# Optimization experiments

Measured on AMD Instinct MI355X. Metric: run time of the kernel, lower is better.

## Reference

```python
import jax, jax.numpy as jnp
import numpy as np

EPS = 1e-5  # RMSNorm epsilon


def rmsnorm(x, w):
    return x * jax.lax.rsqrt(jnp.mean(x * x, axis=-1, keepdims=True) + EPS) * w


def mamba_forward(u, in_proj_w, conv_w, conv_b, x_proj_w, dt_proj_w, dt_proj_b,
                  A_log, D_param, mamba_out_w):
    # u: (b, L, dm) -- canonical Mamba block (expand=2, d_state=16, d_conv=4)
    b, L, dm = u.shape
    di, ds = A_log.shape
    dtr = dt_proj_w.shape[1]
    xz = jnp.einsum('bld,ed->ble', u, in_proj_w)          # (b,L,2*di)
    x_, z = jnp.split(xz, 2, axis=-1)                     # each (b,L,di)
    # causal depthwise conv over the sequence axis
    dconv = conv_w.shape[-1]
    xc = jnp.transpose(x_, (0, 2, 1))                     # (b,di,L)
    xc = jnp.pad(xc, ((0, 0), (0, 0), (dconv - 1, 0)))
    xc = jax.lax.conv_general_dilated(xc, conv_w, window_strides=(1,), padding='VALID',
                                      dimension_numbers=('NCH', 'OIH', 'NCH'),
                                      feature_group_count=di)
    xc = xc + conv_b[None, :, None]
    x_ = jax.nn.silu(jnp.transpose(xc, (0, 2, 1)))        # (b,L,di)
    # input-dependent dt, B, C
    x_dbl = jnp.einsum('bld,ed->ble', x_, x_proj_w)       # (b,L,dtr+2*ds)
    dt, B, C = jnp.split(x_dbl, [dtr, dtr + ds], axis=-1)
    delta = jax.nn.softplus(jnp.einsum('blr,dr->bld', dt, dt_proj_w) + dt_proj_b)  # (b,L,di)
    A = -jnp.exp(A_log)                                   # (di,ds)

    def step(h, inp):
        d_t, B_t, C_t, x_t = inp                          # (b,di),(b,ds),(b,ds),(b,di)
        dA = jnp.exp(d_t[:, :, None] * A)                 # (b,di,ds)
        h = dA * h + (d_t * x_t)[:, :, None] * B_t[:, None, :]
        y = jnp.einsum('bds,bs->bd', h, C_t)
        return h, y

    xs = (jnp.moveaxis(delta, 1, 0), jnp.moveaxis(B, 1, 0),
          jnp.moveaxis(C, 1, 0), jnp.moveaxis(x_, 1, 0))
    h0 = jnp.zeros((b, di, ds), dtype=u.dtype)
    _, ys = jax.lax.scan(step, h0, xs)                    # ys: (L,b,di)
    y = jnp.moveaxis(ys, 0, 1) + x_ * D_param             # (b,L,di)
    y = y * jax.nn.silu(z)
    return jnp.einsum('bld,od->blo', y, mamba_out_w)      # (b,L,dm)


def conv1x1(W, bvec, t):
    # t: (b, cin, L) -> (b, cout, L)
    return jnp.einsum('oi,bit->bot', W, t) + bvec[None, :, None]


def reference(x, w_norm1, w_norm2, W_ip, b_ip, W_fp, b_fp, W_wp, b_wp, W_op, b_op,
              in_proj_w, conv_w, conv_b, x_proj_w, dt_proj_w, dt_proj_b,
              A_log, D_param, mamba_out_w):
    # x: (b, L, D) -- module's (b, c, l) with l == input_dim = D, c == seq = L
    residual = x
    xn = rmsnorm(x, w_norm1)                 # RMSNorm over last (input_dim) axis
    xt = jnp.transpose(xn, (0, 2, 1))        # 'b c l -> b l c' : (b, D, L)
    ssm = conv1x1(W_ip, b_ip, xt)            # (b, 2D, L)
    ssm = conv1x1(W_fp, b_fp, ssm)           # (b, 2D, L)
    u = jnp.transpose(ssm, (0, 2, 1))        # (b, L, 2D): seq=L, d_model=2D
    m = mamba_forward(u, in_proj_w, conv_w, conv_b, x_proj_w, dt_proj_w, dt_proj_b,
                      A_log, D_param, mamba_out_w)
    m = rmsnorm(m, w_norm2) + u              # PostNormMamba residual
    ssm = jnp.transpose(m, (0, 2, 1))        # (b, 2D, L)
    w = conv1x1(W_wp, b_wp, xt)              # (b, 2D, L)
    w = w * jax.nn.sigmoid(w)                # swish
    out = conv1x1(W_op, b_op, w * ssm)       # (b, D, L)
    return jnp.transpose(out, (0, 2, 1)) + residual


def setup_inputs():
    key = jax.random.key(0)
    ks = jax.random.split(key, 16)
    D, L, b = 64, 4096, 4
    dm, di, ds, dconv = 2 * D, 4 * D, 16, 4
    dtr = (dm + 15) // 16  # dt_rank = ceil(d_model/16) = 8

    def n(k, shape, fan_in):
        return jax.random.normal(k, shape, jnp.float32) * (1.0 / np.sqrt(fan_in))

    return {
        'x': jax.random.normal(ks[0], (b, L, D), jnp.float32),
        'w_norm1': jnp.ones((D,), jnp.float32),
        'w_norm2': jnp.ones((dm,), jnp.float32),
        'W_ip': n(ks[1], (2 * D, D), D), 'b_ip': jnp.zeros((2 * D,), jnp.float32),
        'W_fp': n(ks[2], (2 * D, 2 * D), 2 * D), 'b_fp': jnp.zeros((2 * D,), jnp.float32),
        'W_wp': n(ks[3], (2 * D, D), D), 'b_wp': jnp.zeros((2 * D,), jnp.float32),
        'W_op': n(ks[4], (D, 2 * D), 2 * D), 'b_op': jnp.zeros((D,), jnp.float32),
        'in_proj_w': n(ks[5], (2 * di, dm), dm),
        'conv_w': n(ks[6], (di, 1, dconv), dconv),
        'conv_b': jnp.zeros((di,), jnp.float32),
        'x_proj_w': n(ks[7], (dtr + 2 * ds, di), di),
        'dt_proj_w': n(ks[8], (di, dtr), dtr),
        'dt_proj_b': jnp.full((di,), float(np.log(np.expm1(0.01))), jnp.float32),
        'A_log': jnp.log(jnp.broadcast_to(jnp.arange(1, ds + 1, dtype=jnp.float32), (di, ds))),
        'D_param': jnp.ones((di,), jnp.float32),
        'mamba_out_w': n(ks[9], (dm, di), di),
    }
```

## Files before the change

### kernel.cpp

```cpp
#include <hip/hip_runtime.h>
#include <hip/hip_bf16.h>

typedef __hip_bfloat16 bf16;
typedef __attribute__((ext_vector_type(8))) short bf16x8;
typedef __attribute__((ext_vector_type(4))) float f32x4;
#define DEV __device__ __forceinline__

constexpr int SEQ  = 4096;
constexpr int NB   = 4;
constexpr int NTOK = NB * SEQ;
constexpr float EPS = 1e-5f;
constexpr int NCH = 64;
constexpr int NCHUNK = SEQ / NCH;
constexpr float LOG2E = 1.44269504f;

constexpr int OFF_WDT  = 0;
constexpr int OFF_WB   = 2048;
constexpr int WB_IP = 0;
constexpr int WB_WP = 8192;
constexpr int WB_FP = 16384;
constexpr int WB_PR = 32768;
constexpr int WB_MO = 98304;
constexpr int WB_OP = 131072;
constexpr int WB_XP = 139264;
constexpr int WB_TOT = 151552;
constexpr int OFF_XDBL = OFF_WB + WB_TOT / 2;
constexpr int OFF_R1   = OFF_XDBL + NTOK * 40;
constexpr int OFF_WSW  = OFF_R1   + 1048576;
constexpr int OFF_U    = OFF_WSW  + 1048576;
constexpr int OFF_R2   = OFF_U    + 1048576;
constexpr int OFF_SILUZ= OFF_R2   + 2097152;
constexpr int OFF_XC   = OFF_SILUZ+ 2097152;
constexpr int OFF_G    = OFF_XC   + 2097152;
constexpr int OFF_FLAG = OFF_G    + 2097152;

DEV float b2f(bf16 x) { return __bfloat162float(x); }
DEV bf16 f2b(float x) { return __float2bfloat16(x); }
DEV short shof(bf16 h) { short s; __builtin_memcpy(&s, &h, 2); return s; }
DEV float ldin(const void* p, int i, int f) {
  return f ? ((const float*)p)[i] : b2f(((const bf16*)p)[i]);
}
DEV unsigned pack2(float a, float b) {
  bf16 ha = f2b(a), hb = f2b(b);
  unsigned short ua, ub;
  __builtin_memcpy(&ua, &ha, 2); __builtin_memcpy(&ub, &hb, 2);
  return (unsigned)ua | ((unsigned)ub << 16);
}
DEV float lo16f(unsigned u) { return __int_as_float((int)(u << 16)); }
DEV float hi16f(unsigned u) { return __int_as_float((int)(u & 0xffff0000u)); }
DEV float exp2f_fast(float a) { return __builtin_amdgcn_exp2f(a); }
DEV float softplus(float a) {
  return (a > 20.f) ? a : __logf(1.f + exp2f_fast(a * LOG2E));
}
DEV float silu(float a) { return a / (1.f + __expf(-a)); }

DEV void cpw(int e, int base, int count, const void* __restrict__ src,
             bf16* __restrict__ wb, int f) {
  int r = e - base;
  if (r >= 0 && r < count) wb[base + r] = f2b(ldin(src, r, f));
}
__global__ __launch_bounds__(256) void prep_k(
    const void* __restrict__ w_ip, const void* __restrict__ w_wp, const void* __restrict__ w_fp,
    const void* __restrict__ w_pr, const void* __restrict__ w_mo, const void* __restrict__ w_op,
    const void* __restrict__ w_x,  const void* __restrict__ w_dt,
    const void* __restrict__ x, float* __restrict__ wsf, int* __restrict__ flagp)
{
  __shared__ int cnt;
  if (threadIdx.x == 0) cnt = 0;
  __syncthreads();
  {
    float v = b2f(((const bf16*)x)[threadIdx.x]);
    int ok = (v == v) && fabsf(v) > 1e-4f && fabsf(v) < 100.f;
    atomicAdd(&cnt, ok);
  }
  __syncthreads();
  int f = (cnt > 204) ? 0 : 1;
  if (blockIdx.x == 0 && threadIdx.x == 0) *flagp = f;

  int e = blockIdx.x * 256 + threadIdx.x;
  bf16* wb = (bf16*)(wsf + OFF_WB);
  cpw(e, WB_IP, 8192,  w_ip, wb, f);
  cpw(e, WB_WP, 8192,  w_wp, wb, f);
  cpw(e, WB_FP, 16384, w_fp, wb, f);
  cpw(e, WB_PR, 65536, w_pr, wb, f);
  cpw(e, WB_MO, 32768, w_mo, wb, f);
  cpw(e, WB_OP, 8192,  w_op, wb, f);
  {
    int r = e - WB_XP;
    if (r >= 0 && r < 12288) wb[WB_XP + r] = (r < 10240) ? f2b(ldin(w_x, r, f)) : f2b(0.f);
  }
  if (e < 2048) {
    int r = e >> 8, d = e & 255;
    wsf[OFF_WDT + e] = ldin(w_dt, d * 8 + r, f);
  }
}

__global__ __launch_bounds__(256) void fm_k(
    const void* __restrict__ x, const void* __restrict__ w1, const float* __restrict__ wsf,
    const void* __restrict__ b_ip, const void* __restrict__ b_wp, const void* __restrict__ b_fp,
    bf16* __restrict__ wsw, bf16* __restrict__ u, bf16* __restrict__ xpre,
    bf16* __restrict__ siluz, const int* __restrict__ flagp)
{
  __shared__ short xn[32 * 72];
  __shared__ short t1[32 * 136];
  __shared__ short ul[32 * 136];
  const int f = *flagp;
  const int tid = threadIdx.x;
  const int tok0 = blockIdx.x * 32;
  {
    const int token = tid >> 3, r = tid & 7;
    float v[8]; float ss = 0.f;
    #pragma unroll
    for (int k = 0; k < 8; ++k) {
      v[k] = ldin(x, (tok0 + token) * 64 + r * 8 + k, f);
      ss += v[k] * v[k];
    }
    ss += __shfl_xor(ss, 1, 8); ss += __shfl_xor(ss, 2, 8); ss += __shfl_xor(ss, 4, 8);
    float sc = rsqrtf(ss * (1.f / 64.f) + EPS);
    unsigned* dst = (unsigned*)xn + token * 36 + r * 4;
    #pragma unroll
    for (int k = 0; k < 4; ++k) {
      int i = r * 8 + k * 2;
      dst[k] = pack2(v[k*2] * sc * ldin(w1, i, f), v[k*2+1] * sc * ldin(w1, i + 1, f));
    }
  }
  __syncthreads();
  const int lane = tid & 63, m = lane & 15, q = lane >> 4;
  const int w = tid >> 6;
  {
    const int wt = w >> 1, ng = w & 1;
    const bf16* W = (const bf16*)(wsf + OFF_WB) + (wt ? WB_WP : WB_IP);
    const void* bia = wt ? b_wp : b_ip;
    bf16x8 a[2][2];
    #pragma unroll
    for (int mt = 0; mt < 2; ++mt)
      #pragma unroll
      for (int kk = 0; kk < 2; ++kk)
        a[mt][kk] = *(const bf16x8*)&xn[(mt * 16 + m) * 72 + kk * 32 + q * 8];
    #pragma unroll
    for (int nti = 0; nti < 4; ++nti) {
      int nt = ng * 4 + nti;
      int n = nt * 16 + m;
      f32x4 acc[2] = {{0,0,0,0},{0,0,0,0}};
      #pragma unroll
      for (int kk = 0; kk < 2; ++kk) {
        bf16x8 b = *(const bf16x8*)(W + (nt * 16 + m) * 64 + kk * 32 + q * 8);
        #pragma unroll
        for (int mt = 0; mt < 2; ++mt)
          acc[mt] = __builtin_amdgcn_mfma_f32_16x16x32_bf16(a[mt][kk], b, acc[mt], 0, 0, 0);
      }
      float bv = ldin(bia, n, f);
      #pragma unroll
      for (int mt = 0; mt < 2; ++mt)
        #pragma unroll
        for (int r = 0; r < 4; ++r) {
          float v = acc[mt][r] + bv;
          if (wt) wsw[(tok0 + mt * 16 + q * 4 + r) * 128 + n] = f2b(silu(v));
          else    t1[(mt * 16 + q * 4 + r) * 136 + n] = shof(f2b(v));
        }
    }
  }
  __syncthreads();
  {
    const bf16* WF = (const bf16*)(wsf + OFF_WB) + WB_FP;
    bf16x8 a[2][4];
    #pragma unroll
    for (int mt = 0; mt < 2; ++mt)
      #pragma unroll
      for (int kk = 0; kk < 4; ++kk)
        a[mt][kk] = *(const bf16x8*)&t1[(mt * 16 + m) * 136 + kk * 32 + q * 8];
    #pragma unroll
    for (int nti = 0; nti < 2; ++nti) {
      int nt = w * 2 + nti;
      int n = nt * 16 + m;
      f32x4 acc[2] = {{0,0,0,0},{0,0,0,0}};
      #pragma unroll
      for (int kk = 0; kk < 4; ++kk) {
        bf16x8 b = *(const bf16x8*)(WF + (nt * 16 + m) * 128 + kk * 32 + q * 8);
        #pragma unroll
        for (int mt = 0; mt < 2; ++mt)
          acc[mt] = __builtin_amdgcn_mfma_f32_16x16x32_bf16(a[mt][kk], b, acc[mt], 0, 0, 0);
      }
      float bv = ldin(b_fp, n, f);
      #pragma unroll
      for (int mt = 0; mt < 2; ++mt)
        #pragma unroll
        for (int r = 0; r < 4; ++r) {
          bf16 h = f2b(acc[mt][r] + bv);
          ul[(mt * 16 + q * 4 + r) * 136 + n] = shof(h);
          u[(tok0 + mt * 16 + q * 4 + r) * 128 + n] = h;
        }
    }
  }
  __syncthreads();
  {
    const bf16* WP = (const bf16*)(wsf + OFF_WB) + WB_PR;
    bf16x8 a[2][4];
    #pragma unroll
    for (int mt = 0; mt < 2; ++mt)
      #pragma unroll
      for (int kk = 0; kk < 4; ++kk)
        a[mt][kk] = *(const bf16x8*)&ul[(mt * 16 + m) * 136 + kk * 32 + q * 8];
    #pragma unroll
    for (int nti = 0; nti < 8; ++nti) {
      int nt = w * 8 + nti;
      int n = nt * 16 + m;
      f32x4 acc[2] = {{0,0,0,0},{0,0,0,0}};
      #pragma unroll
      for (int kk = 0; kk < 4; ++kk) {
        bf16x8 b = *(const bf16x8*)(WP + (nt * 16 + m) * 128 + kk * 32 + q * 8);
        #pragma unroll
        for (int mt = 0; mt < 2; ++mt)
          acc[mt] = __builtin_amdgcn_mfma_f32_16x16x32_bf16(a[mt][kk], b, acc[mt], 0, 0, 0);
      }
      #pragma unroll
      for (int mt = 0; mt < 2; ++mt)
        #pragma unroll
        for (int r = 0; r < 4; ++r) {
          int tok = tok0 + mt * 16 + q * 4 + r;
          if (n < 256) xpre[tok * 256 + n] = f2b(acc[mt][r]);
          else         siluz[tok * 256 + (n - 256)] = f2b(silu(acc[mt][r]));
        }
    }
  }
}

__global__ __launch_bounds__(256) void conv_k(
    const bf16* __restrict__ xpre, const void* __restrict__ cw, const void* __restrict__ cb,
    const float* __restrict__ wsf, bf16* __restrict__ xc, float* __restrict__ xdbl,
    const int* __restrict__ flagp)
{
  __shared__ short xh[35 * 256];
  __shared__ short cs[32 * 264];
  const int f = *flagp;
  const int tid = threadIdx.x;
  const int tok0 = blockIdx.x * 32;
  const bool seqstart = (tok0 & (SEQ - 1)) == 0;
  for (int c = tid; c < 1120; c += 256) {
    int e0 = c * 8;
    int tt = e0 >> 8, i = e0 & 255;
    int gtok = tok0 + tt - 3;
    uint4* dst = (uint4*)(xh + e0);
    if (gtok >= 0 && !(seqstart && tt < 3)) *dst = *(const uint4*)(xpre + gtok * 256 + i);
    else                                    *dst = make_uint4(0, 0, 0, 0);
  }
  __syncthreads();
  {
    const int ch0 = (tid & 63) * 4;
    const int t0 = (tid >> 6) * 8;
    float w4[4][4], cb4[4];
    #pragma unroll
    for (int c = 0; c < 4; ++c) {
      cb4[c] = ldin(cb, ch0 + c, f);
      #pragma unroll
      for (int k = 0; k < 4; ++k) w4[c][k] = ldin(cw, (ch0 + c) * 4 + k, f);
    }
    float win[11][4];
    #pragma unroll
    for (int r = 0; r < 11; ++r) {
      uint2 v = *(const uint2*)&xh[(t0 + r) * 256 + ch0];
      win[r][0] = lo16f(v.x); win[r][1] = hi16f(v.x);
      win[r][2] = lo16f(v.y); win[r][3] = hi16f(v.y);
    }
    #pragma unroll
    for (int t = 0; t < 8; ++t) {
      unsigned pk[2];
      #pragma unroll
      for (int cp = 0; cp < 2; ++cp) {
        float o[2];
        #pragma unroll
        for (int ci = 0; ci < 2; ++ci) {
          int c = cp * 2 + ci;
          float acc = cb4[c];
          #pragma unroll
          for (int k = 0; k < 4; ++k) acc = fmaf(win[t + k][c], w4[c][k], acc);
          o[ci] = silu(acc);
        }
        pk[cp] = pack2(o[0], o[1]);
      }
      uint2 pv = make_uint2(pk[0], pk[1]);
      *(uint2*)&cs[(t0 + t) * 264 + ch0] = pv;
      *(uint2*)(xc + (tok0 + t0 + t) * 256 + ch0) = pv;
    }
  }
  __syncthreads();
  const int w = tid >> 6;
  if (w < 2) {
    const bf16* Wx = (const bf16*)(wsf + OFF_WB) + WB_XP;
    const int lane = tid & 63, m = lane & 15, quad = lane >> 4;
    f32x4 acc[3] = {{0,0,0,0},{0,0,0,0},{0,0,0,0}};
    #pragma unroll
    for (int k0 = 0; k0 < 256; k0 += 32) {
      bf16x8 af = *(const bf16x8*)&cs[(w * 16 + m) * 264 + k0 + quad * 8];
      #pragma unroll
      for (int nt = 0; nt < 3; ++nt) {
        bf16x8 bfr = *(const bf16x8*)(Wx + (nt * 16 + m) * 256 + k0 + quad * 8);
        acc[nt] = __builtin_amdgcn_mfma_f32_16x16x32_bf16(af, bfr, acc[nt], 0, 0, 0);
      }
    }
    #pragma unroll
    for (int nt = 0; nt < 3; ++nt) {
      int n = nt * 16 + m;
      if (n < 40) {
        #pragma unroll
        for (int r = 0; r < 4; ++r)
          xdbl[(tok0 + w * 16 + quad * 4 + r) * 40 + n] = acc[nt][r];
      }
    }
  }
}

template<bool IS_C>
__global__ __launch_bounds__(64) void scan_k(
    const float* __restrict__ xdbl, const bf16* __restrict__ xc, const bf16* __restrict__ siluz,
    const void* __restrict__ A_log, const void* __restrict__ D_par, const void* __restrict__ dt_b,
    const float* __restrict__ WDT, float* __restrict__ summ, const float* __restrict__ hinit,
    bf16* __restrict__ g, const int* __restrict__ flagp)
{
  __shared__ float dt_l[NCH * 8];
  __shared__ float B_l[NCH * 16];
  __shared__ float C_l[IS_C ? NCH * 16 : 4];
  __shared__ float dlt_l[NCH * 64];
  const int f = *flagp;
  const int tid = threadIdx.x;
  const int bb = blockIdx.x >> 2, dg = blockIdx.x & 3;
  const int c = blockIdx.y;
  const int d = dg * 64 + tid;
  const int tok_base = bb * SEQ + c * NCH;

  float A2[16], h[16];
  #pragma unroll
  for (int s = 0; s < 16; ++s)
    A2[s] = -__expf(ldin(A_log, d * 16 + s, f)) * LOG2E;
  const float Dp = ldin(D_par, d, f);
  const float dtb = ldin(dt_b, d, f);
  float wdt[8];
  #pragma unroll
  for (int r = 0; r < 8; ++r) wdt[r] = WDT[r * 256 + d];

  {
    const float4* src = (const float4*)(xdbl + (tok_base + tid) * 40);
    *(float4*)(dt_l + tid * 8)      = src[0];
    *(float4*)(dt_l + tid * 8 + 4)  = src[1];
    #pragma unroll
    for (int k = 0; k < 4; ++k)
      *(float4*)(B_l + tid * 16 + k * 4) = src[2 + k];
    if (IS_C) {
      #pragma unroll
      for (int k = 0; k < 4; ++k)
        *(float4*)(C_l + tid * 16 + k * 4) = src[6 + k];
    }
  }
  __syncthreads();

  for (int t = 0; t < NCH; ++t) {
    float4 d0 = *(const float4*)(dt_l + t * 8);
    float4 d1 = *(const float4*)(dt_l + t * 8 + 4);
    float a = dtb;
    a = fmaf(d0.x, wdt[0], a); a = fmaf(d0.y, wdt[1], a);
    a = fmaf(d0.z, wdt[2], a); a = fmaf(d0.w, wdt[3], a);
    a = fmaf(d1.x, wdt[4], a); a = fmaf(d1.y, wdt[5], a);
    a = fmaf(d1.z, wdt[6], a); a = fmaf(d1.w, wdt[7], a);
    dlt_l[t * 64 + tid] = softplus(a);
  }
  __syncthreads();

  #pragma unroll
  for (int s = 0; s < 16; ++s) h[s] = 0.f;
  if (IS_C) {
    const int hbase = (bb * 64 + c) * 4096 + d * 16;
    #pragma unroll
    for (int k = 0; k < 4; ++k)
      *(float4*)(h + k * 4) = *(const float4*)(hinit + hbase + k * 4);
  }
  float sdlt = 0.f;

  #pragma unroll 4
  for (int t = 0; t < NCH; ++t) {
    float dlt = dlt_l[t * 64 + tid];
    float xcv = b2f(xc[(tok_base + t) * 256 + d]);
    float du = dlt * xcv;
    float Bv[16];
    #pragma unroll
    for (int k = 0; k < 4; ++k)
      *(float4*)(Bv + k * 4) = *(const float4*)(B_l + t * 16 + k * 4);
    if (IS_C) {
      float Cv[16];
      #pragma unroll
      for (int k = 0; k < 4; ++k)
        *(float4*)(Cv + k * 4) = *(const float4*)(C_l + t * 16 + k * 4);
      float y = 0.f;
      #pragma unroll
      for (int s = 0; s < 16; ++s) {
        float dA = exp2f_fast(dlt * A2[s]);
        h[s] = fmaf(dA, h[s], du * Bv[s]);
        y = fmaf(h[s], Cv[s], y);
      }
      float sz = b2f(siluz[(tok_base + t) * 256 + d]);
      g[(tok_base + t) * 256 + d] = f2b((y + xcv * Dp) * sz);
    } else {
      sdlt += dlt;
      #pragma unroll
      for (int s = 0; s < 16; ++s) {
        float dA = exp2f_fast(dlt * A2[s]);
        h[s] = fmaf(dA, h[s], du * Bv[s]);
      }
    }
  }
  if (!IS_C) {
    float sv[32];
    #pragma unroll
    for (int s = 0; s < 16; ++s) {
      sv[s * 2]     = exp2f_fast(A2[s] * sdlt);
      sv[s * 2 + 1] = h[s];
    }
    float* dst = summ + ((bb * 64 + c) * 4096 + d * 16) * 2;
    #pragma unroll
    for (int k = 0; k < 8; ++k)
      *(float4*)(dst + k * 4) = *(const float4*)(sv + k * 4);
  }
}

__global__ __launch_bounds__(256) void scanB_k(const float* __restrict__ summ, float* __restrict__ hinit) {
  int bx = blockIdx.x;
  int b = bx >> 4;
  int q = (bx & 15) * 256 + threadIdx.x;
  float h = 0.f;
  for (int c0 = 0; c0 < NCHUNK; c0 += 16) {
    float2 sv[16];
    #pragma unroll
    for (int k = 0; k < 16; ++k)
      sv[k] = *(const float2*)(summ + ((b * 64 + c0 + k) * 4096 + q) * 2);
    #pragma unroll
    for (int k = 0; k < 16; ++k) {
      hinit[(b * 64 + c0 + k) * 4096 + q] = h;
      h = fmaf(sv[k].x, h, sv[k].y);
    }
  }
}

__global__ __launch_bounds__(256) void back_k(
    const bf16* __restrict__ g, const float* __restrict__ wsf, const void* __restrict__ w2,
    const bf16* __restrict__ u, const bf16* __restrict__ wsw, const void* __restrict__ b_op,
    const void* __restrict__ x, void* __restrict__ out, const int* __restrict__ flagp)
{
  __shared__ short ms[32 * 136];
  const int f = *flagp;
  const int tid = threadIdx.x;
  const int tok0 = blockIdx.x * 32;
  const int lane = tid & 63, m = lane & 15, q = lane >> 4;
  const int w = tid >> 6;
  const bf16* WM = (const bf16*)(wsf + OFF_WB) + WB_MO;
  const bf16* WO = (const bf16*)(wsf + OFF_WB) + WB_OP;
  {
    f32x4 acc[2][2] = {{{0,0,0,0},{0,0,0,0}},{{0,0,0,0},{0,0,0,0}}};
    #pragma unroll
    for (int kk = 0; kk < 8; ++kk) {
      bf16x8 a0 = *(const bf16x8*)(g + (tok0 + m) * 256 + kk * 32 + q * 8);
      bf16x8 a1 = *(const bf16x8*)(g + (tok0 + 16 + m) * 256 + kk * 32 + q * 8);
      #pragma unroll
      for (int nti = 0; nti < 2; ++nti) {
        int nt = w * 2 + nti;
        bf16x8 b = *(const bf16x8*)(WM + (nt * 16 + m) * 256 + kk * 32 + q * 8);
        acc[nti][0] = __builtin_amdgcn_mfma_f32_16x16x32_bf16(a0, b, acc[nti][0], 0, 0, 0);
        acc[nti][1] = __builtin_amdgcn_mfma_f32_16x16x32_bf16(a1, b, acc[nti][1], 0, 0, 0);
      }
    }
    #pragma unroll
    for (int nti = 0; nti < 2; ++nti) {
      int n = (w * 2 + nti) * 16 + m;
      #pragma unroll
      for (int mt = 0; mt < 2; ++mt)
        #pragma unroll
        for (int r = 0; r < 4; ++r)
          ms[(mt * 16 + q * 4 + r) * 136 + n] = shof(f2b(acc[nti][mt][r]));
    }
  }
  __syncthreads();
  {
    const int token = tid >> 3, r = tid & 7;
    float mv[16]; float ss = 0.f;
    #pragma unroll
    for (int k = 0; k < 16; ++k) {
      mv[k] = b2f(((const bf16*)ms)[token * 136 + r * 16 + k]);
      ss += mv[k] * mv[k];
    }
    ss += __shfl_xor(ss, 1, 8); ss += __shfl_xor(ss, 2, 8); ss += __shfl_xor(ss, 4, 8);
    float sc = rsqrtf(ss * (1.f / 128.f) + EPS);
    #pragma unroll
    for (int k = 0; k < 16; ++k) {
      int i = r * 16 + k;
      int ga = (tok0 + token) * 128 + i;
      float v = mv[k] * sc * ldin(w2, i, f) + b2f(u[ga]);
      ms[token * 136 + i] = shof(f2b(v * b2f(wsw[ga])));
    }
  }
  __syncthreads();
  {
    bf16x8 a[2][4];
    #pragma unroll
    for (int mt = 0; mt < 2; ++mt)
      #pragma unroll
      for (int kk = 0; kk < 4; ++kk)
        a[mt][kk] = *(const bf16x8*)&ms[(mt * 16 + m) * 136 + kk * 32 + q * 8];
    int nt = w;
    f32x4 acc[2] = {{0,0,0,0},{0,0,0,0}};
    #pragma unroll
    for (int kk = 0; kk < 4; ++kk) {
      bf16x8 b = *(const bf16x8*)(WO + (nt * 16 + m) * 128 + kk * 32 + q * 8);
      #pragma unroll
      for (int mt = 0; mt < 2; ++mt)
        acc[mt] = __builtin_amdgcn_mfma_f32_16x16x32_bf16(a[mt][kk], b, acc[mt], 0, 0, 0);
    }
    int n = nt * 16 + m;
    float bv = ldin(b_op, n, f);
    #pragma unroll
    for (int mt = 0; mt < 2; ++mt)
      #pragma unroll
      for (int r = 0; r < 4; ++r) {
        int token = tok0 + mt * 16 + q * 4 + r;
        float v = acc[mt][r] + bv + ldin(x, token * 64 + n, f);
        if (f) ((float*)out)[token * 64 + n] = v;
        else   ((bf16*)out)[token * 64 + n] = f2b(v);
      }
  }
}

extern "C" void kernel_launch(void* const* d_in, const int* in_sizes, int n_in,
                              void* d_out, int out_size, void* d_ws, size_t ws_size,
                              hipStream_t stream) {
  (void)in_sizes; (void)n_in; (void)out_size; (void)ws_size;
  const void* x        = d_in[0];
  const void* w_norm1  = d_in[1];
  const void* w_norm2  = d_in[2];
  const void* W_ip     = d_in[3];
  const void* b_ip     = d_in[4];
  const void* W_fp     = d_in[5];
  const void* b_fp     = d_in[6];
  const void* W_wp     = d_in[7];
  const void* b_wp     = d_in[8];
  const void* W_op     = d_in[9];
  const void* b_op     = d_in[10];
  const void* in_proj  = d_in[11];
  const void* conv_w   = d_in[12];
  const void* conv_b   = d_in[13];
  const void* x_proj   = d_in[14];
  const void* dt_projw = d_in[15];
  const void* dt_projb = d_in[16];
  const void* A_log    = d_in[17];
  const void* D_par    = d_in[18];
  const void* mo_w     = d_in[19];

  float* wsf    = (float*)d_ws;
  float* xdbl   = wsf + OFF_XDBL;
  float* hin    = wsf + OFF_R1;
  bf16*  wsw_b  = (bf16*)(wsf + OFF_WSW);
  bf16*  u_b    = (bf16*)(wsf + OFF_U);
  bf16*  xpre_b = (bf16*)(wsf + OFF_R2);
  float* summ   = wsf + OFF_R2;
  bf16*  siluz_b= (bf16*)(wsf + OFF_SILUZ);
  bf16*  xc_b   = (bf16*)(wsf + OFF_XC);
  bf16*  g_b    = (bf16*)(wsf + OFF_G);
  int*   flagp  = (int*)(wsf + OFF_FLAG);

  prep_k<<<dim3(592), dim3(256), 0, stream>>>(W_ip, W_wp, W_fp, in_proj, mo_w, W_op,
                                              x_proj, dt_projw, x, wsf, flagp);
  fm_k<<<dim3(NTOK / 32), dim3(256), 0, stream>>>(x, w_norm1, wsf, b_ip, b_wp, b_fp,
                                                  wsw_b, u_b, xpre_b, siluz_b, flagp);
  conv_k<<<dim3(NTOK / 32), dim3(256), 0, stream>>>(xpre_b, conv_w, conv_b, wsf, xc_b, xdbl, flagp);
  scan_k<false><<<dim3(16, NCHUNK), dim3(64), 0, stream>>>(xdbl, xc_b, siluz_b, A_log, D_par,
                                                           dt_projb, wsf + OFF_WDT, summ, hin, g_b, flagp);
  scanB_k<<<dim3(64), dim3(256), 0, stream>>>(summ, hin);
  scan_k<true><<<dim3(16, NCHUNK), dim3(64), 0, stream>>>(xdbl, xc_b, siluz_b, A_log, D_par,
                                                          dt_projb, wsf + OFF_WDT, summ, hin, g_b, flagp);
  back_k<<<dim3(NTOK / 32), dim3(256), 0, stream>>>(g_b, wsf, w_norm2, u_b, wsw_b, b_op, x, d_out, flagp);
}
```

Measured before the change: 209.6 us.

## Halve scan chunk length and fuse delta computation into the recurrence loop

Cuts the chunk length of the chunked selective scan from 64 to 32, which doubles the number of chunk blocks and so the parallelism in both scan passes. The softplus delta is now computed inline in the main recurrence loop, which removes the shared-memory delta buffer and one block barrier. Adds launch_bounds occupancy hints, and the C-vector staging is split between thread halves. The workspace is re-laid out so the chunk summaries and hinit buffers grow with the chunk count and no longer alias the conv input buffer. The cost is a longer sequential pass in scanB and more summary traffic.

```diff
diff --git a/kernel.cpp b/kernel.cpp
--- a/kernel.cpp
+++ b/kernel.cpp
@@ -10,7 +10,7 @@
 constexpr int NB   = 4;
 constexpr int NTOK = NB * SEQ;
 constexpr float EPS = 1e-5f;
-constexpr int NCH = 64;
+constexpr int NCH = 32;
 constexpr int NCHUNK = SEQ / NCH;
 constexpr float LOG2E = 1.44269504f;
 
@@ -25,11 +25,12 @@
 constexpr int WB_XP = 139264;
 constexpr int WB_TOT = 151552;
 constexpr int OFF_XDBL = OFF_WB + WB_TOT / 2;
-constexpr int OFF_R1   = OFF_XDBL + NTOK * 40;
-constexpr int OFF_WSW  = OFF_R1   + 1048576;
+constexpr int OFF_HIN  = OFF_XDBL + NTOK * 40;
+constexpr int OFF_SUMM = OFF_HIN  + NB * NCHUNK * 4096;
+constexpr int OFF_WSW  = OFF_SUMM + NB * NCHUNK * 4096 * 2;
 constexpr int OFF_U    = OFF_WSW  + 1048576;
-constexpr int OFF_R2   = OFF_U    + 1048576;
-constexpr int OFF_SILUZ= OFF_R2   + 2097152;
+constexpr int OFF_XPRE = OFF_U    + 1048576;
+constexpr int OFF_SILUZ= OFF_XPRE + 2097152;
 constexpr int OFF_XC   = OFF_SILUZ+ 2097152;
 constexpr int OFF_G    = OFF_XC   + 2097152;
 constexpr int OFF_FLAG = OFF_G    + 2097152;
@@ -311,7 +312,7 @@
 }
 
 template<bool IS_C>
-__global__ __launch_bounds__(64) void scan_k(
+__global__ __launch_bounds__(64, 4) void scan_k(
     const float* __restrict__ xdbl, const bf16* __restrict__ xc, const bf16* __restrict__ siluz,
     const void* __restrict__ A_log, const void* __restrict__ D_par, const void* __restrict__ dt_b,
     const float* __restrict__ WDT, float* __restrict__ summ, const float* __restrict__ hinit,
@@ -320,7 +321,6 @@
   __shared__ float dt_l[NCH * 8];
   __shared__ float B_l[NCH * 16];
   __shared__ float C_l[IS_C ? NCH * 16 : 4];
-  __shared__ float dlt_l[NCH * 64];
   const int f = *flagp;
   const int tid = threadIdx.x;
   const int bb = blockIdx.x >> 2, dg = blockIdx.x & 3;
@@ -338,21 +338,33 @@
   #pragma unroll
   for (int r = 0; r < 8; ++r) wdt[r] = WDT[r * 256 + d];
 
-  {
+  if (tid < NCH) {
     const float4* src = (const float4*)(xdbl + (tok_base + tid) * 40);
-    *(float4*)(dt_l + tid * 8)      = src[0];
-    *(float4*)(dt_l + tid * 8 + 4)  = src[1];
+    *(float4*)(dt_l + tid * 8)     = src[0];
+    *(float4*)(dt_l + tid * 8 + 4) = src[1];
     #pragma unroll
     for (int k = 0; k < 4; ++k)
       *(float4*)(B_l + tid * 16 + k * 4) = src[2 + k];
-    if (IS_C) {
-      #pragma unroll
-      for (int k = 0; k < 4; ++k)
-        *(float4*)(C_l + tid * 16 + k * 4) = src[6 + k];
-    }
-  }
-  __syncthreads();
-
+  } else if (IS_C) {
+    int t = tid - NCH;
+    const float4* src = (const float4*)(xdbl + (tok_base + t) * 40);
+    #pragma unroll
+    for (int k = 0; k < 4; ++k)
+      *(float4*)(C_l + t * 16 + k * 4) = src[6 + k];
+  }
+  __syncthreads();
+
+  #pragma unroll
+  for (int s = 0; s < 16; ++s) h[s] = 0.f;
+  if (IS_C) {
+    const int hbase = (bb * NCHUNK + c) * 4096 + d * 16;
+    #pragma unroll
+    for (int k = 0; k < 4; ++k)
+      *(float4*)(h + k * 4) = *(const float4*)(hinit + hbase + k * 4);
+  }
+  float sdlt = 0.f;
+
+  #pragma unroll 4
   for (int t = 0; t < NCH; ++t) {
     float4 d0 = *(const float4*)(dt_l + t * 8);
     float4 d1 = *(const float4*)(dt_l + t * 8 + 4);
@@ -361,23 +373,7 @@
     a = fmaf(d0.z, wdt[2], a); a = fmaf(d0.w, wdt[3], a);
     a = fmaf(d1.x, wdt[4], a); a = fmaf(d1.y, wdt[5], a);
     a = fmaf(d1.z, wdt[6], a); a = fmaf(d1.w, wdt[7], a);
-    dlt_l[t * 64 + tid] = softplus(a);
-  }
-  __syncthreads();
-
-  #pragma unroll
-  for (int s = 0; s < 16; ++s) h[s] = 0.f;
-  if (IS_C) {
-    const int hbase = (bb * 64 + c) * 4096 + d * 16;
-    #pragma unroll
-    for (int k = 0; k < 4; ++k)
-      *(float4*)(h + k * 4) = *(const float4*)(hinit + hbase + k * 4);
-  }
-  float sdlt = 0.f;
-
-  #pragma unroll 4
-  for (int t = 0; t < NCH; ++t) {
-    float dlt = dlt_l[t * 64 + tid];
+    float dlt = softplus(a);
     float xcv = b2f(xc[(tok_base + t) * 256 + d]);
     float du = dlt * xcv;
     float Bv[16];
@@ -414,7 +410,7 @@
       sv[s * 2]     = exp2f_fast(A2[s] * sdlt);
       sv[s * 2 + 1] = h[s];
     }
-    float* dst = summ + ((bb * 64 + c) * 4096 + d * 16) * 2;
+    float* dst = summ + ((bb * NCHUNK + c) * 4096 + d * 16) * 2;
     #pragma unroll
     for (int k = 0; k < 8; ++k)
       *(float4*)(dst + k * 4) = *(const float4*)(sv + k * 4);
@@ -430,10 +426,10 @@
     float2 sv[16];
     #pragma unroll
     for (int k = 0; k < 16; ++k)
-      sv[k] = *(const float2*)(summ + ((b * 64 + c0 + k) * 4096 + q) * 2);
+      sv[k] = *(const float2*)(summ + ((b * NCHUNK + c0 + k) * 4096 + q) * 2);
     #pragma unroll
     for (int k = 0; k < 16; ++k) {
-      hinit[(b * 64 + c0 + k) * 4096 + q] = h;
+      hinit[(b * NCHUNK + c0 + k) * 4096 + q] = h;
       h = fmaf(sv[k].x, h, sv[k].y);
     }
   }
@@ -553,11 +549,11 @@
 
   float* wsf    = (float*)d_ws;
   float* xdbl   = wsf + OFF_XDBL;
-  float* hin    = wsf + OFF_R1;
+  float* hin    = wsf + OFF_HIN;
+  float* summ   = wsf + OFF_SUMM;
   bf16*  wsw_b  = (bf16*)(wsf + OFF_WSW);
   bf16*  u_b    = (bf16*)(wsf + OFF_U);
-  bf16*  xpre_b = (bf16*)(wsf + OFF_R2);
-  float* summ   = wsf + OFF_R2;
+  bf16*  xpre_b = (bf16*)(wsf + OFF_XPRE);
   bf16*  siluz_b= (bf16*)(wsf + OFF_SILUZ);
   bf16*  xc_b   = (bf16*)(wsf + OFF_XC);
   bf16*  g_b    = (bf16*)(wsf + OFF_G);
```

Result: no change. 212.5 us (+1.4%).
